# Kernel tuning notes

Hardware: AMD Instinct MI355X
Metric: run time of the kernel (lower is better)

## Reference

```python
import jax, jax.numpy as jnp
import numpy as np
import math


def _interp_linear(x, t_out):
    # x: [B, D, Lin] -> [B, D, t_out]; matches torch F.interpolate(mode='linear', align_corners=False)
    lin = x.shape[-1]
    pos = (jnp.arange(t_out, dtype=jnp.float32) + 0.5) * (lin / t_out) - 0.5
    pos = jnp.clip(pos, 0.0, lin - 1.0)
    lo = jnp.floor(pos).astype(jnp.int32)
    hi = jnp.minimum(lo + 1, lin - 1)
    w = pos - lo.astype(jnp.float32)
    return x[..., lo] * (1.0 - w) + x[..., hi] * w


def _forward(x, in_w, in_b, gq_w, gq_b, gk_w, gk_b, gv_w, gv_b, go_w, go_b, curv,
             wav0, wav1, wav2, wav3, wrec_w, wrec_b,
             te1_w, te1_b, te2_w, te2_b, td1_w, td1_b, td2_w, td2_b, bd_w, bd_b,
             cc_w, cc_b, ln_g, ln_b, mm1_w, mm1_b, mm2_w, mm2_b,
             dn1_w, dn1_b, dn2_w, dn2_b, dn3_w, dn3_b, out_w, out_b,
             noise_sched, noise):
    B, T, _ = x.shape
    L, H = curv.shape
    D = in_w.shape[1]
    hd = D // H
    dn = ('NCH', 'OIH', 'NCH')
    h = x @ in_w + in_b
    total_loss = jnp.float32(0.0)
    wavs = [wav0, wav1, wav2, wav3]
    for l in range(L):  # static small layer loop
        # ---- GeometricAttention (vectorized hyperbolic-distance softmax) ----
        q = (h @ gq_w[l] + gq_b[l]).reshape(B, T, H, hd)
        k = (h @ gk_w[l] + gk_b[l]).reshape(B, T, H, hd)
        v = (h @ gv_w[l] + gv_b[l]).reshape(B, T, H, hd)
        c = jnp.abs(curv[l]) + 1e-8                       # [H]
        cb = c[None, :, None, None]
        qn = jnp.einsum('bthd,bthd->bht', q, q)           # [B,H,T]
        kn = jnp.einsum('bthd,bthd->bht', k, k)
        qk = jnp.einsum('bihd,bjhd->bhij', q, k)          # [B,H,T,T]
        d2 = jnp.maximum(qn[:, :, :, None] + kn[:, :, None, :] - 2.0 * qk, 0.0)
        denom = jnp.maximum((1.0 - cb * qn[:, :, :, None]) * (1.0 - cb * kn[:, :, None, :]), 1e-5)
        arg = jnp.maximum(1.0 + cb * (2.0 * d2) / denom, 1.00001)
        dist = jnp.arccosh(arg) / jnp.sqrt(cb)
        attn = jax.nn.softmax(-dist, axis=-1)             # temperature = 1.0
        geom = jnp.einsum('bhij,bjhd->bihd', attn, v).reshape(B, T, D) @ go_w[l] + go_b[l]
        # ---- WaveletTransform ----
        xf = h.transpose(0, 2, 1)                          # [B,D,T]
        decomps = []
        for i, wv in enumerate(wavs):
            filt = jax.nn.softmax(wv[l], axis=-1)          # [D,K]
            K = filt.shape[-1]
            dec = jax.lax.conv_general_dilated(xf, filt[:, None, :], (1,), [(K - 1, 0)],
                                               feature_group_count=D, dimension_numbers=dn)
            dec = dec[:, :, ::2 ** (i + 1)]
            decomps.append(_interp_linear(dec, T))
        comb = jnp.concatenate(decomps, axis=1).transpose(0, 2, 1)  # [B,T,4D]
        wave = comb @ wrec_w[l] + wrec_b[l]
        # ---- TopologicalLayer ----
        tf = jax.nn.relu(h @ te1_w[l] + te1_b[l]) @ te2_w[l] + te2_b[l]
        topo = h + (jax.nn.relu(tf @ td1_w[l] + td1_b[l]) @ td2_w[l] + td2_b[l])
        bd = tf @ bd_w[l] + bd_b[l]
        total_loss = total_loss + jnp.mean(jax.nn.relu(bd[..., 0] - bd[..., 1] + 0.1))
        # ---- CausalConvolution (kernel 3, dilation 2**l) ----
        dil = 2 ** l
        pad = 2 * dil
        cc = jax.lax.conv_general_dilated(h.transpose(0, 2, 1), cc_w[l], (1,), [(pad, 0)],
                                          rhs_dilation=(dil,), dimension_numbers=dn)
        cc = (cc + cc_b[l][None, :, None]).transpose(0, 2, 1)
        # ---- combine + LayerNorm (dropout is identity in eval) ----
        s = geom + wave + topo + cc
        mu = jnp.mean(s, axis=-1, keepdims=True)
        var = jnp.var(s, axis=-1, keepdims=True)
        h = (s - mu) / jnp.sqrt(var + 1e-5) * ln_g + ln_b
    # ---- manifold mixer (T > 1 branch) ----
    last = h[:, -1]
    pen = h[:, -2]
    mix = jnp.tanh(jnp.concatenate([last, pen], axis=-1) @ mm1_w + mm1_b) @ mm2_w + mm2_b
    cur = last + mix
    # ---- diffusion refinement ----
    half = D // 2
    emb_f = jnp.exp(jnp.arange(half, dtype=jnp.float32) * (-math.log(10000.0) / (half - 1)))
    S = noise.shape[0]
    for t in range(S):  # static diffusion_steps=10
        noisy = cur + noise[t] * noise_sched[t]
        te = jnp.full((B, 1), float(t), dtype=jnp.float32) * emb_f[None, :]
        temb = jnp.concatenate([jnp.sin(te), jnp.cos(te)], axis=-1)  # [B,D]
        di = jnp.concatenate([noisy, temb], axis=-1)
        npred = jax.nn.silu(jax.nn.silu(di @ dn1_w + dn1_b) @ dn2_w + dn2_b) @ dn3_w + dn3_b
        cur = cur - npred * noise_sched[t]
    pred = cur @ out_w + out_b
    return pred, total_loss


def setup_inputs() -> dict:
    key = jax.random.key(0)
    B, T, Din, D, L, H, P, S = 16, 256, 384, 512, 6, 8, 64, 10
    ctr = [0]
    def rn(shape, s=0.05):
        ctr[0] += 1
        return jax.random.normal(jax.random.fold_in(key, ctr[0]), shape, jnp.float32) * s
    d = {}
    d['x'] = rn((B, T, Din), 1.0)
    d['in_w'] = rn((Din, D)); d['in_b'] = rn((D,), 0.01)
    for nm in ['gq', 'gk', 'gv', 'go']:
        d[nm + '_w'] = rn((L, D, D)); d[nm + '_b'] = rn((L, D), 0.01)
    d['curv'] = rn((L, H), 1.0)
    for i in range(4):
        d['wav%d' % i] = rn((L, D, 2 ** (i + 2)), 1.0)
    d['wrec_w'] = rn((L, 4 * D, D)); d['wrec_b'] = rn((L, D), 0.01)
    d['te1_w'] = rn((L, D, P)); d['te1_b'] = rn((L, P), 0.01)
    d['te2_w'] = rn((L, P, P)); d['te2_b'] = rn((L, P), 0.01)
    d['td1_w'] = rn((L, P, D)); d['td1_b'] = rn((L, D), 0.01)
    d['td2_w'] = rn((L, D, D)); d['td2_b'] = rn((L, D), 0.01)
    d['bd_w'] = rn((L, P, 2)); d['bd_b'] = rn((L, 2), 0.01)
    d['cc_w'] = rn((L, D, D, 3)); d['cc_b'] = rn((L, D), 0.01)
    d['ln_g'] = jnp.ones((D,), jnp.float32); d['ln_b'] = jnp.zeros((D,), jnp.float32)
    d['mm1_w'] = rn((2 * D, D)); d['mm1_b'] = rn((D,), 0.01)
    d['mm2_w'] = rn((D, D)); d['mm2_b'] = rn((D,), 0.01)
    d['dn1_w'] = rn((2 * D, D)); d['dn1_b'] = rn((D,), 0.01)
    d['dn2_w'] = rn((D, D)); d['dn2_b'] = rn((D,), 0.01)
    d['dn3_w'] = rn((D, D)); d['dn3_b'] = rn((D,), 0.01)
    d['out_w'] = rn((D, Din)); d['out_b'] = rn((Din,), 0.01)
    d['noise_sched'] = jnp.linspace(0.1, 0.9, S).astype(jnp.float32)
    d['noise'] = rn((S, B, D), 1.0)
    return d


def reference(x, in_w, in_b, gq_w, gq_b, gk_w, gk_b, gv_w, gv_b, go_w, go_b, curv,
              wav0, wav1, wav2, wav3, wrec_w, wrec_b,
              te1_w, te1_b, te2_w, te2_b, td1_w, td1_b, td2_w, td2_b, bd_w, bd_b,
              cc_w, cc_b, ln_g, ln_b, mm1_w, mm1_b, mm2_w, mm2_b,
              dn1_w, dn1_b, dn2_w, dn2_b, dn3_w, dn3_b, out_w, out_b,
              noise_sched, noise):
    return _forward(x, in_w, in_b, gq_w, gq_b, gk_w, gk_b, gv_w, gv_b, go_w, go_b, curv,
                    wav0, wav1, wav2, wav3, wrec_w, wrec_b,
                    te1_w, te1_b, te2_w, te2_b, td1_w, td1_b, td2_w, td2_b, bd_w, bd_b,
                    cc_w, cc_b, ln_g, ln_b, mm1_w, mm1_b, mm2_w, mm2_b,
                    dn1_w, dn1_b, dn2_w, dn2_b, dn3_w, dn3_b, out_w, out_b,
                    noise_sched, noise)
```

## Files before the change

kernel.cpp:

```cpp
#include <hip/hip_runtime.h>
#include <hip/hip_bf16.h>
#include <math.h>

#define BB 16
#define TT 256
#define DIN 384
#define DD 512
#define LL 6
#define HH 8
#define PP 64
#define SS 10
#define BT (BB*TT)

enum { ACT_NONE=0, ACT_RELU=1, ACT_TANH=2, ACT_SILU=3, ACT_RELU_TAIL=4 };

typedef __attribute__((ext_vector_type(8))) short bf16x8;
typedef __attribute__((ext_vector_type(4))) float f32x4;
typedef __hip_bfloat16 bh16;

typedef const __attribute__((address_space(1))) void gvoid_t;
typedef __attribute__((address_space(3))) void lvoid_t;
__device__ __forceinline__ void gload16(const void* g, void* l) {
    __builtin_amdgcn_global_load_lds((gvoid_t*)g, (lvoid_t*)l, 16, 0, 0);
}
// ... 416 lines not shown
            }
    #pragma unroll
    for (int off = 1; off < 16; off <<= 1)
        #pragma unroll
        for (int fm = 0; fm < 2; ++fm)
            #pragma unroll
            for (int r = 0; r < 4; ++r)
                rmax[fm][r] = fmaxf(rmax[fm][r], __shfl_xor(rmax[fm][r], off));
    if ((lane & 15) == 0)
        #pragma unroll
        for (int fm = 0; fm < 2; ++fm)
            #pragma unroll
            for (int r = 0; r < 4; ++r)
                redA[wn][wm*32 + fm*16 + (lane>>4)*4 + r] = rmax[fm][r];
    __syncthreads();
    #pragma unroll
    for (int fm = 0; fm < 2; ++fm)
        #pragma unroll
        for (int r = 0; r < 4; ++r)
            rmax[fm][r] = fmaxf(rmax[fm][r], redA[wn ^ 1][wm*32 + fm*16 + (lane>>4)*4 + r]);
    float rsum[2][4];
    #pragma unroll
    for (int fm = 0; fm < 2; ++fm)
        #pragma unroll
        for (int r = 0; r < 4; ++r) rsum[fm][r] = 0.f;
    #pragma unroll
    for (int fm = 0; fm < 2; ++fm)
        #pragma unroll
        for (int fn = 0; fn < 8; ++fn)
            #pragma unroll
            for (int r = 0; r < 4; ++r) {
                float e = expf(acc[fm][fn][r] - rmax[fm][r]);
                acc[fm][fn][r] = e;
                rsum[fm][r] += e;
            }
    #pragma unroll
    for (int off = 1; off < 16; off <<= 1)
        #pragma unroll
        for (int fm = 0; fm < 2; ++fm)
            #pragma unroll
            for (int r = 0; r < 4; ++r)
                rsum[fm][r] += __shfl_xor(rsum[fm][r], off);
    if ((lane & 15) == 0)
        #pragma unroll
        for (int fm = 0; fm < 2; ++fm)
            #pragma unroll
            for (int r = 0; r < 4; ++r)
                redB[wn][wm*32 + fm*16 + (lane>>4)*4 + r] = rsum[fm][r];
    __syncthreads();
    float pinv[2][4];
    #pragma unroll
    for (int fm = 0; fm < 2; ++fm)
        #pragma unroll
        for (int r = 0; r < 4; ++r)
            pinv[fm][r] = 1.f / (rsum[fm][r] + redB[wn ^ 1][wm*32 + fm*16 + (lane>>4)*4 + r]);

    f32x4 acc2[2][2];
    #pragma unroll
    for (int i = 0; i < 2; ++i)
        #pragma unroll
        for (int j = 0; j < 2; ++j) acc2[i][j] = (f32x4){0.f,0.f,0.f,0.f};

    const bh16* vbase = qkv + 1024 + hh * 64;
    for (int kt = 0; kt < 4; ++kt) {
        __syncthreads();
        if (wn == (kt >> 1)) {
            int fnb = (kt & 1) * 4;
            #pragma unroll
            for (int fm = 0; fm < 2; ++fm)
                #pragma unroll
                for (int fnl = 0; fnl < 4; ++fnl)
                    #pragma unroll
                    for (int r = 0; r < 4; ++r) {
                        int rowl = wm*32 + fm*16 + (lane>>4)*4 + r;
                        int kl = fnl*16 + (lane & 15);
                        float p = acc[fm][fnb + fnl][r] * pinv[fm][r];
                        Ps[(rowl*8 + ((kl >> 3) ^ (rowl & 7)))*8 + (kl & 7)] = __float2bfloat16(p);
                    }
        }
        #pragma unroll
        for (int j = 0; j < 2; ++j) {
            int c = threadIdx.x + j*256;
            int tr = c >> 3, chk = c & 7;
            bf16x8 v = *(const bf16x8*)(vbase + (size_t)(b*256 + kt*64 + tr)*1600 + chk*8);
            *(bf16x8*)(&Vst[tr*72 + chk*8]) = v;
        }
        __syncthreads();
        #pragma unroll
        for (int j = 0; j < 2; ++j) {
            int c = threadIdx.x + j*256;
            int col = c & 63, chk = c >> 6;
            bf16x8 v;
            #pragma unroll
            for (int e = 0; e < 8; ++e)
                v[e] = (short)Vst[(chk*8 + e)*72 + col];
            Bv[col*8 + (chk ^ (col & 7))] = v;
        }
        __syncthreads();

        bf16x8 pa[2][2], vb[2][2];
        #pragma unroll
        for (int fm = 0; fm < 2; ++fm) {
            int row = wm*32 + fm*16 + (lane & 15);
            #pragma unroll
            for (int ks = 0; ks < 2; ++ks)
                pa[fm][ks] = ((bf16x8*)Ps)[row*8 + ((ks*4 + (lane>>4)) ^ (row & 7))];
        }
        #pragma unroll
        for (int fn = 0; fn < 2; ++fn) {
            int col = wn*32 + fn*16 + (lane & 15);
            #pragma unroll
            for (int ks = 0; ks < 2; ++ks)
                vb[fn][ks] = Bv[col*8 + ((ks*4 + (lane>>4)) ^ (col & 7))];
        }
        #pragma unroll
        for (int ks = 0; ks < 2; ++ks)
            #pragma unroll
            for (int fm = 0; fm < 2; ++fm)
                #pragma unroll
                for (int fn = 0; fn < 2; ++fn)
                    acc2[fm][fn] = __builtin_amdgcn_mfma_f32_16x16x32_bf16(
                        pa[fm][ks], vb[fn][ks], acc2[fm][fn], 0, 0, 0);
    }

    #pragma unroll
    for (int fm = 0; fm < 2; ++fm)
        #pragma unroll
        for (int fn = 0; fn < 2; ++fn)
            #pragma unroll
            for (int r = 0; r < 4; ++r) {
                int rowl = wm*32 + fm*16 + (lane>>4)*4 + r;
                int col = wn*32 + fn*16 + (lane & 15);
                gmb[((size_t)(b*256 + rh*64 + rowl))*512 + hh*64 + col] =
                    __float2bfloat16(acc2[fm][fn][r]);
            }
}

__global__ __launch_bounds__(256) void fgemm_kernel(
    const bh16* __restrict__ A0, const bh16* __restrict__ A1,
    const bh16* __restrict__ A2, const bh16* __restrict__ A3,
    const bh16* __restrict__ B0, const bh16* __restrict__ B1,
    const bh16* __restrict__ B2, const bh16* __restrict__ B3,
    const float* __restrict__ bias,
    float* __restrict__ Cf0, float* __restrict__ Cf1,
    float* __restrict__ Cf2, float* __restrict__ Cf3,
    int dil, const bh16* __restrict__ zp)
{
    __shared__ bf16x8 As[128*8];
    __shared__ bf16x8 Bs[64*8];

    int bx = blockIdx.x, by = blockIdx.y;
    xcd_swizzle_always(bx, by);
    const int zz = blockIdx.z;
    const int ktlo = zz * 18;
    const int kthi = ktlo + 18;

    const int tid  = threadIdx.x;
    const int lane = tid & 63, w = tid >> 6;
    const int wm = w >> 1, wn = w & 1;
    const int row0 = by * 128, col0 = bx * 64;

    f32x4 acc[4][2];
    #pragma unroll
    for (int i = 0; i < 4; ++i)
        #pragma unroll
        for (int j = 0; j < 2; ++j) acc[i][j] = (f32x4){0.f,0.f,0.f,0.f};

    for (int kt = ktlo; kt < kthi; ++kt) {
        const bh16* Aseg; const bh16* Bseg;
        int ldas, ldbs, k0, mask_sh, addr_sh;
        if (kt < 8) {
            Aseg = A0; Bseg = B0; ldas = 512; ldbs = 512;
            k0 = kt << 6; mask_sh = 0; addr_sh = 0;
        } else if (kt < 40) {
            Aseg = A1; Bseg = B1; ldas = 2048; ldbs = 2048;
            k0 = (kt - 8) << 6; mask_sh = 0; addr_sh = 0;
        } else if (kt < 48) {
            Aseg = A2; Bseg = B2; ldas = 512; ldbs = 512;
            k0 = (kt - 40) << 6; mask_sh = 0; addr_sh = 0;
        } else {
            int kl = kt - 48, tap = kl >> 3;
            Aseg = A3; Bseg = B3; ldas = 512; ldbs = 1536;
            k0 = kl << 6;
            mask_sh = (2 - tap) * dil;
            addr_sh = mask_sh + tap;
        }
        #pragma unroll
        for (int j = 0; j < 4; ++j) {
            int c = ((w*4 + j) << 6) + lane;
            int row = c >> 3, chk = c & 7;
            int schk = chk ^ (row & 7);
            int grow = row0 + row;
            const bh16* src = ((grow & 255) >= mask_sh)
                ? (Aseg + (size_t)(grow - addr_sh)*ldas + k0 + schk*8) : zp;
            gload16(src, &As[(w*4 + j) * 64]);
        }
        #pragma unroll
        for (int j = 0; j < 2; ++j) {
            int c = ((w*2 + j) << 6) + lane;
            int row = c >> 3, chk = c & 7;
            int schk = chk ^ (row & 7);
            int gcol = col0 + row;
            gload16(Bseg + (size_t)gcol*ldbs + k0 + schk*8, &Bs[(w*2 + j) * 64]);
        }
        asm volatile("s_waitcnt vmcnt(0)" ::: "memory");
        __syncthreads();

        bf16x8 a[4][2], b[2][2];
        #pragma unroll
        for (int fm = 0; fm < 4; ++fm) {
            int row = wm*64 + fm*16 + (lane & 15);
            #pragma unroll
            for (int ks = 0; ks < 2; ++ks)
                a[fm][ks] = As[row*8 + ((ks*4 + (lane>>4)) ^ (row & 7))];
        }
        #pragma unroll
        for (int fn = 0; fn < 2; ++fn) {
            int col = wn*32 + fn*16 + (lane & 15);
            #pragma unroll
            for (int ks = 0; ks < 2; ++ks)
                b[fn][ks] = Bs[col*8 + ((ks*4 + (lane>>4)) ^ (col & 7))];
        }
        #pragma unroll
        for (int ks = 0; ks < 2; ++ks)
            #pragma unroll
            for (int fm = 0; fm < 4; ++fm)
                #pragma unroll
                for (int fn = 0; fn < 2; ++fn)
                    acc[fm][fn] = __builtin_amdgcn_mfma_f32_16x16x32_bf16(
                        a[fm][ks], b[fn][ks], acc[fm][fn], 0, 0, 0);
        __syncthreads();
    }

    float* Cf = (zz == 0) ? Cf0 : (zz == 1) ? Cf1 : (zz == 2) ? Cf2 : Cf3;
    #pragma unroll
    for (int fm = 0; fm < 4; ++fm) {
        #pragma unroll
        for (int fn = 0; fn < 2; ++fn) {
            int gc = col0 + wn*32 + fn*16 + (lane & 15);
            float bs = (zz == 0) ? bias[gc] : 0.f;
            #pragma unroll
            for (int r = 0; r < 4; ++r) {
                int gr = row0 + wm*64 + fm*16 + (lane>>4)*4 + r;
                Cf[(size_t)gr*512 + gc] = acc[fm][fn][r] + bs;
            }
        }
    }
}

__global__ __launch_bounds__(256) void hgemm16_kernel(
    const bh16* __restrict__ A, int lda, long aZ,
    const bh16* __restrict__ Bt, int ldb,
    const float* __restrict__ bias,
    const float* __restrict__ pre,
    float* __restrict__ Of, bh16* __restrict__ Ob, long oZ,
    int N, int K, int act,
    float* __restrict__ curf, bh16* __restrict__ curb,
    const float* __restrict__ scaleptr)
{
    const int z = blockIdx.z;
    A += (long)z * aZ;
    const int lane = threadIdx.x & 63, w = threadIdx.x >> 6;
    const int col0 = blockIdx.x * 64 + w * 16;
    const int ar = lane & 15;
    const int koff = (lane >> 4) * 8;
    const bh16* arow = A + (size_t)ar * lda + koff;
    const bh16* brow = Bt + (size_t)(col0 + ar) * ldb + koff;
    f32x4 acc = {0.f, 0.f, 0.f, 0.f};
    const int nkt = K >> 5;
    for (int kt0 = 0; kt0 < nkt; kt0 += 8) {
        bf16x8 av[8], bv[8];
        #pragma unroll
        for (int j = 0; j < 8; ++j) {
            av[j] = *(const bf16x8*)(arow + (size_t)(kt0 + j) * 32);
            bv[j] = *(const bf16x8*)(brow + (size_t)(kt0 + j) * 32);
        }
        #pragma unroll
        for (int j = 0; j < 8; ++j)
            acc = __builtin_amdgcn_mfma_f32_16x16x32_bf16(av[j], bv[j], acc, 0, 0, 0);
    }
    const int col = col0 + ar;
    float bs = bias ? bias[col] : 0.f;
    float sc = scaleptr ? *scaleptr : 0.f;
    #pragma unroll
    for (int r = 0; r < 4; ++r) {
        int row = (lane >> 4) * 4 + r;
        float v = acc[r] + bs;
        if (pre) v += pre[(size_t)row * N + col];
        if (act == ACT_SILU)      v = v / (1.f + expf(-v));
        else if (act == ACT_TANH) v = tanhf(v);
        if (curf) {
            size_t o = (size_t)row * 512 + col;
            float nc = curf[o] - v * sc;
            curf[o] = nc;
            curb[o] = __float2bfloat16(nc);
        } else {
            size_t o = (size_t)z * oZ + (size_t)row * N + col;
            if (Of) Of[o] = v;
            if (Ob) Ob[o] = __float2bfloat16(v);
        }
    }
}

__device__ __forceinline__ f32x4 hslice(const bh16* A, int lda, const bh16* Bt, int ldb,
                                        int col0, int K, int lane)
{
    const int ar = lane & 15;
    const int koff = (lane >> 4) * 8;
    const bh16* arow = A + (size_t)ar * lda + koff;
    const bh16* brow = Bt + (size_t)(col0 + ar) * ldb + koff;
    f32x4 acc = {0.f, 0.f, 0.f, 0.f};
    const int nkt = K >> 5;
    for (int kt0 = 0; kt0 < nkt; kt0 += 8) {
        bf16x8 av[8], bv[8];
        #pragma unroll
        for (int j = 0; j < 8; ++j) {
            av[j] = *(const bf16x8*)(arow + (size_t)(kt0 + j) * 32);
            bv[j] = *(const bf16x8*)(brow + (size_t)(kt0 + j) * 32);
        }
        #pragma unroll
        for (int j = 0; j < 8; ++j)
            acc = __builtin_amdgcn_mfma_f32_16x16x32_bf16(av[j], bv[j], acc, 0, 0, 0);
    }
    return acc;
}

__device__ __forceinline__ void headbar(int* ctr, int* bar)
{
    __threadfence();
    __syncthreads();
    if (threadIdx.x == 0) {
        __hip_atomic_fetch_add(ctr, 1, __ATOMIC_ACQ_REL, __HIP_MEMORY_SCOPE_AGENT);
        *bar += 8;
        while (__hip_atomic_load(ctr, __ATOMIC_ACQUIRE, __HIP_MEMORY_SCOPE_AGENT) < *bar)
            __builtin_amdgcn_s_sleep(8);
    }
    __syncthreads();
    __threadfence();
}

__global__ __launch_bounds__(256) void head_kernel(
    const float* __restrict__ h,
    const bh16* __restrict__ mm1T, const float* __restrict__ mm1b,
    const bh16* __restrict__ mm2T, const float* __restrict__ mm2b,
    const bh16* __restrict__ dn1T,
    const bh16* __restrict__ dn2T, const float* __restrict__ dn2b,
    const bh16* __restrict__ dn3T, const float* __restrict__ dn3b,
    const bh16* __restrict__ outT, const float* __restrict__ outb,
    const float* __restrict__ pre1, const float* __restrict__ nsched,
    bh16* __restrict__ tmb16, float* __restrict__ curf, bh16* __restrict__ cur16,
    bh16* __restrict__ d1b16, bh16* __restrict__ d2b16,
    float* __restrict__ out, int* __restrict__ ctr)
{
    __shared__ __align__(16) bh16 catL[16 * 1032];
    const int bx = blockIdx.x;
    const int tid = threadIdx.x;
    const int lane = tid & 63, w = tid >> 6;
    int bar = 0;

    for (int e = tid; e < 16 * 1024; e += 256) {
        int k = e & 1023, b = e >> 10;
        float v = (k < 512) ? h[((size_t)b * TT + 255) * DD + k]
                            : h[((size_t)b * TT + 254) * DD + (k - 512)];
        catL[b * 1032 + k] = __float2bfloat16(v);
    }
    __syncthreads();

    const int col0 = bx * 64 + w * 16;
    const int colr = col0 + (lane & 15);

    {
        f32x4 acc = hslice((const bh16*)catL, 1032, mm1T, 1024, col0, 1024, lane);
        float bs = mm1b[colr];
        #pragma unroll
        for (int r = 0; r < 4; ++r) {
            int row = (lane >> 4) * 4 + r;
            tmb16[(size_t)row * 512 + colr] = __float2bfloat16(tanhf(acc[r] + bs));
        }
    }
    headbar(ctr, &bar);
    {
        f32x4 acc = hslice(tmb16, 512, mm2T, 512, col0, 512, lane);
        float bs = mm2b[colr];
        #pragma unroll
        for (int r = 0; r < 4; ++r) {
            int row = (lane >> 4) * 4 + r;
            float cv = h[((size_t)row * TT + 255) * DD + colr] + acc[r] + bs;
            curf[(size_t)row * 512 + colr] = cv;
            cur16[(size_t)row * 512 + colr] = __float2bfloat16(cv);
        }
    }
    headbar(ctr, &bar);
    for (int t = 0; t < SS; ++t) {
        float sc = nsched[t];
        {
            f32x4 acc = hslice(cur16, 512, dn1T, 1024, col0, 512, lane);
            #pragma unroll
            for (int r = 0; r < 4; ++r) {
                int row = (lane >> 4) * 4 + r;
                float v = acc[r] + pre1[(size_t)t * 8192 + row * 512 + colr];
                v = v / (1.f + expf(-v));
                d1b16[(size_t)row * 512 + colr] = __float2bfloat16(v);
            }
        }
        headbar(ctr, &bar);
        {
            f32x4 acc = hslice(d1b16, 512, dn2T, 512, col0, 512, lane);
            float bs = dn2b[colr];
            #pragma unroll
            for (int r = 0; r < 4; ++r) {
                int row = (lane >> 4) * 4 + r;
                float v = acc[r] + bs;
                v = v / (1.f + expf(-v));
                d2b16[(size_t)row * 512 + colr] = __float2bfloat16(v);
            }
        }
        headbar(ctr, &bar);
        {
            f32x4 acc = hslice(d2b16, 512, dn3T, 512, col0, 512, lane);
            float bs = dn3b[colr];
            #pragma unroll
            for (int r = 0; r < 4; ++r) {
                int row = (lane >> 4) * 4 + r;
                size_t o = (size_t)row * 512 + colr;
                float nc = curf[o] - (acc[r] + bs) * sc;
                curf[o] = nc;
                cur16[o] = __float2bfloat16(nc);
            }
        }
        headbar(ctr, &bar);
    }
    if (bx < 6) {
        f32x4 acc = hslice(cur16, 512, outT, 512, col0, 512, lane);
        float bs = outb[colr];
        #pragma unroll
        for (int r = 0; r < 4; ++r) {
            int row = (lane >> 4) * 4 + r;
            out[(size_t)row * 384 + colr] = acc[r] + bs;
        }
    }
}

__global__ __launch_bounds__(256) void wave4_kernel(const bh16* __restrict__ hb,
                                                    const float* __restrict__ wav0,
                                                    const float* __restrict__ wav1,
                                                    const float* __restrict__ wav2,
                                                    const float* __restrict__ wav3,
                                                    int l,
                                                    bh16* __restrict__ comb)
{
    __shared__ float dtile[66 * 64];
    __shared__ float ftile[32 * 64];
    const int dblk = blockIdx.x;
    const int iy = blockIdx.y;
    const int b = blockIdx.z;
    const int i = iy >> 1, thalf = iy & 1;
    const int Karr[4] = {4, 8, 16, 32};
    const int K = Karr[i], sv = 2 << i, Ti = 128 >> i;
    const int tid = threadIdx.x;
    const int dbase = dblk * 64;
    if (tid < 64) {
        const float* wsrc = (i == 0) ? wav0 : (i == 1) ? wav1 : (i == 2) ? wav2 : wav3;
        const float* row = wsrc + ((size_t)l * DD + dbase + tid) * K;
        float mx = -1e30f;
        for (int k = 0; k < K; ++k) mx = fmaxf(mx, row[k]);
        float s = 0.f;
        for (int k = 0; k < K; ++k) { float e = expf(row[k] - mx); ftile[k*64 + tid] = e; s += e; }
        float inv = 1.f / s;
        for (int k = 0; k < K; ++k) ftile[k*64 + tid] *= inv;
    }
    const float invsv = 1.f / (float)sv;
    const int t0 = thalf * 128;
    float p0 = ((float)t0 + 0.5f) * invsv - 0.5f;
    p0 = fminf(fmaxf(p0, 0.f), (float)(Ti - 1));
    const int jbase = (int)p0;
    float p1 = ((float)(t0 + 127) + 0.5f) * invsv - 0.5f;
    p1 = fminf(fmaxf(p1, 0.f), (float)(Ti - 1));
    const int him = min((int)p1 + 1, Ti - 1);
    const int jcount = him - jbase + 1;
    __syncthreads();
    const bh16* hcol = hb + (size_t)b * (TT * DD) + dbase;
    for (int e = tid; e < jcount * 64; e += 256) {
        int jl = e >> 6, d0 = e & 63;
        int j = jbase + jl;
        int tb = j * sv - (K - 1);
        float acc = 0.f;
        #pragma unroll 4
        for (int k = 0; k < K; ++k) {
            int t = tb + k;
            if (t >= 0)
                acc += b2f(*(const unsigned short*)(hcol + (size_t)t * DD + d0)) * ftile[k * 64 + d0];
        }
        dtile[jl * 64 + d0] = acc;
    }
    __syncthreads();
    for (int e = tid; e < 128 * 64; e += 256) {
        int tl = e >> 6, d0 = e & 63;
        int t = t0 + tl;
        float pos = ((float)t + 0.5f) * invsv - 0.5f;
        pos = fminf(fmaxf(pos, 0.f), (float)(Ti - 1));
        int lo = (int)pos;
        int hi = min(lo + 1, Ti - 1);
        float w = pos - (float)lo;
        float v = dtile[(lo - jbase) * 64 + d0] * (1.f - w) + dtile[(hi - jbase) * 64 + d0] * w;
        comb[((size_t)b * TT + t) * 2048 + i * 512 + dbase + d0] = __float2bfloat16(v);
    }
}

__global__ __launch_bounds__(256) void add_ln_kernel(const float* __restrict__ s0, const float* __restrict__ s1,
                                                     const float* __restrict__ s2, const float* __restrict__ s3,
                                                     float* __restrict__ h, bh16* __restrict__ hb,
                                                     const float* __restrict__ g, const float* __restrict__ be)
{
    int lane = threadIdx.x & 63, wid = threadIdx.x >> 6;
    size_t row = (size_t)blockIdx.x * 4 + wid;
    const float* sr0 = s0 + row * DD;
    const float* sr1 = s1 + row * DD;
    const float* sr2 = s2 + row * DD;
    const float* sr3 = s3 + row * DD;
    float* hr = h + row * DD;
    bh16* hbr = hb + row * DD;
    float xv[8]; float sum = 0.f;
    #pragma unroll
    for (int u = 0; u < 8; ++u) {
        int c = lane + u * 64;
        xv[u] = sr0[c] + sr1[c] + sr2[c] + sr3[c] + hr[c];
        sum += xv[u];
    }
    #pragma unroll
    for (int off = 32; off; off >>= 1) sum += __shfl_xor(sum, off);
    float mu = sum * (1.f / 512.f);
    float sq = 0.f;
    #pragma unroll
    for (int u = 0; u < 8; ++u) { float d = xv[u] - mu; sq += d * d; }
    #pragma unroll
    for (int off = 32; off; off >>= 1) sq += __shfl_xor(sq, off);
    float rstd = 1.f / sqrtf(sq * (1.f / 512.f) + 1e-5f);
    #pragma unroll
    for (int u = 0; u < 8; ++u) {
        int c = lane + u * 64;
        float v = (xv[u] - mu) * rstd * g[c] + be[c];
        hr[c] = v;
        hbr[c] = __float2bfloat16(v);
    }
}

__global__ __launch_bounds__(256) void wtrans_kernel(const float* __restrict__ W, bh16* __restrict__ Wt,
                                                     int K, int N, long lstride)
{
    int l = blockIdx.z;
    const float* Wl = W + (size_t)l * K * N;
    bh16* Wo = Wt + (size_t)l * lstride;
    __shared__ float tile[32][33];
    int n0 = blockIdx.x * 32, k0 = blockIdx.y * 32;
    int lx = threadIdx.x & 31, ly = threadIdx.x >> 5;
    #pragma unroll
    for (int j = 0; j < 4; ++j) {
        int kk = ly + j * 8;
        tile[kk][lx] = Wl[(size_t)(k0 + kk) * N + n0 + lx];
    }
    __syncthreads();
    #pragma unroll
    for (int j = 0; j < 4; ++j) {
        int nr = ly + j * 8;
        Wo[(size_t)(n0 + nr) * K + k0 + lx] = __float2bfloat16(tile[lx][nr]);
    }
}

__global__ __launch_bounds__(256) void wtrans4_kernel(const float* __restrict__ gq, const float* __restrict__ gk,
                                                      const float* __restrict__ gv, const float* __restrict__ te1,
                                                      bh16* __restrict__ qkvT)
{
    int bxx = blockIdx.x, l = blockIdx.z;
    const float* W; long off; int N; int n0;
    if (bxx < 16)      { W = gq;  off = 0;      N = 512; n0 = bxx * 32; }
    else if (bxx < 32) { W = gk;  off = 262144; N = 512; n0 = (bxx - 16) * 32; }
    else if (bxx < 48) { W = gv;  off = 524288; N = 512; n0 = (bxx - 32) * 32; }
    else               { W = te1; off = 786432; N = 64;  n0 = (bxx - 48) * 32; }
    const float* Wl = W + (size_t)l * 512 * N;
    bh16* Wo = qkvT + (size_t)l * 819200 + off;
    __shared__ float tile[32][33];
    int k0 = blockIdx.y * 32;
    int lx = threadIdx.x & 31, ly = threadIdx.x >> 5;
    #pragma unroll
    for (int j = 0; j < 4; ++j) {
        int kk = ly + j * 8;
        tile[kk][lx] = Wl[(size_t)(k0 + kk) * N + n0 + lx];
    }
    __syncthreads();
    #pragma unroll
    for (int j = 0; j < 4; ++j) {
        int nr = ly + j * 8;
        Wo[(size_t)(n0 + nr) * 512 + k0 + lx] = __float2bfloat16(tile[lx][nr]);
    }
}

__global__ __launch_bounds__(256) void wtransH_kernel(
    const float* __restrict__ mm1w, const float* __restrict__ mm2w,
    const float* __restrict__ dn1w, const float* __restrict__ dn2w,
    const float* __restrict__ dn3w, const float* __restrict__ outw,
    bh16* __restrict__ mm1T, bh16* __restrict__ mm2T, bh16* __restrict__ dn1T,
    bh16* __restrict__ dn2T, bh16* __restrict__ dn3T, bh16* __restrict__ outT)
{
    int bx = blockIdx.x;
    const float* W; bh16* Wo; int K, N, bloc;
    if (bx < 512)       { W = mm1w; Wo = mm1T; K = 1024; N = 512; bloc = bx; }
    else if (bx < 768)  { W = mm2w; Wo = mm2T; K = 512;  N = 512; bloc = bx - 512; }
    else if (bx < 1280) { W = dn1w; Wo = dn1T; K = 1024; N = 512; bloc = bx - 768; }
    else if (bx < 1536) { W = dn2w; Wo = dn2T; K = 512;  N = 512; bloc = bx - 1280; }
    else if (bx < 1792) { W = dn3w; Wo = dn3T; K = 512;  N = 512; bloc = bx - 1536; }
    else                { W = outw; Wo = outT; K = 512;  N = 384; bloc = bx - 1792; }
    int nblk = N / 32;
    int n0 = (bloc % nblk) * 32, k0 = (bloc / nblk) * 32;
    __shared__ float tile[32][33];
    int lx = threadIdx.x & 31, ly = threadIdx.x >> 5;
    #pragma unroll
    for (int j = 0; j < 4; ++j) {
        int kk = ly + j * 8;
        tile[kk][lx] = W[(size_t)(k0 + kk) * N + n0 + lx];
    }
    __syncthreads();
    #pragma unroll
    for (int j = 0; j < 4; ++j) {
        int nr = ly + j * 8;
        Wo[(size_t)(n0 + nr) * K + k0 + lx] = __float2bfloat16(tile[lx][nr]);
    }
}

__global__ __launch_bounds__(256) void ccconv_kernel(const float* __restrict__ ccw, bh16* __restrict__ ccT)
{
    size_t idx = (size_t)blockIdx.x * 256 + threadIdx.x;
    int i = idx & 511; size_t rem = idx >> 9;
    int tap = (int)(rem % 3); rem /= 3;
    int o = (int)(rem & 511); int l = (int)(rem >> 9);
    ccT[idx] = __float2bfloat16(ccw[(((size_t)l*512 + o)*512 + i)*3 + tap]);
}

__global__ __launch_bounds__(256) void qkvbias_kernel(const float* __restrict__ qb_, const float* __restrict__ kb_,
                                                      const float* __restrict__ vb_, const float* __restrict__ t1b_,
                                                      float* __restrict__ ob,
                                                      const float* __restrict__ gob, const float* __restrict__ wrb,
                                                      const float* __restrict__ tdb, const float* __restrict__ ccb,
                                                      float* __restrict__ bsum)
{
    int idx = blockIdx.x * 256 + threadIdx.x;
    if (idx < 6 * 1600) {
        int l = idx / 1600, n = idx % 1600;
        float v = (n < 512) ? qb_[l*512 + n]
                : (n < 1024) ? kb_[l*512 + n - 512]
                : (n < 1536) ? vb_[l*512 + n - 1024]
                : t1b_[l*64 + n - 1536];
        ob[idx] = v;
    }
    if (idx < 6 * 512) {
        bsum[idx] = gob[idx] + wrb[idx] + tdb[idx] + ccb[idx];
    }
}

__global__ __launch_bounds__(256) void convx_kernel(const float* __restrict__ x, bh16* __restrict__ xb)
{
    size_t idx = (size_t)blockIdx.x * 256 + threadIdx.x;
    xb[idx] = __float2bfloat16(x[idx]);
}

__global__ __launch_bounds__(256) void build_E_kernel(const float* __restrict__ noise, const float* __restrict__ sched,
                                                      bh16* __restrict__ E)
{
    int idx = blockIdx.x * 256 + threadIdx.x;
    if (idx >= SS * BB * 1024) return;
    int k = idx & 1023; int rem = idx >> 10; int b = rem & 15; int t = rem >> 4;
    float v;
    if (k < 512) {
        v = sched[t] * noise[((size_t)t * BB + b) * 512 + k];
    } else {
        int j = k - 512;
        const float kfac = -9.210340371976184f / 255.f;
        v = (j < 256) ? sinf((float)t * expf((float)j * kfac))
                      : cosf((float)t * expf((float)(j - 256) * kfac));
    }
    E[idx] = __float2bfloat16(v);
}

__global__ void init_kernel(bh16* zp, float* loss, int* ctr)
{
    int t = threadIdx.x;
    if (t < 64) zp[t] = __float2bfloat16(0.f);
    if (t == 64) *loss = 0.f;
    if (t == 65) *ctr = 0;
}

__global__ void fail_kernel(float* p) { p[0] = 1e30f; }

extern "C" void kernel_launch(void* const* d_in, const int* in_sizes, int n_in,
                              void* d_out, int out_size, void* d_ws, size_t ws_size,
                              hipStream_t stream)
{
    const float* x      = (const float*)d_in[0];
    const float* in_w   = (const float*)d_in[1];
    const float* in_b   = (const float*)d_in[2];
    const float* gq_w   = (const float*)d_in[3];
    const float* gq_b   = (const float*)d_in[4];
    const float* gk_w   = (const float*)d_in[5];
    const float* gk_b   = (const float*)d_in[6];
    const float* gv_w   = (const float*)d_in[7];
    const float* gv_b   = (const float*)d_in[8];
    const float* go_w   = (const float*)d_in[9];
    const float* go_b   = (const float*)d_in[10];
    const float* curv   = (const float*)d_in[11];
    const float* wav0   = (const float*)d_in[12];
    const float* wav1   = (const float*)d_in[13];
    const float* wav2   = (const float*)d_in[14];
    const float* wav3   = (const float*)d_in[15];
    const float* wrec_w = (const float*)d_in[16];
    const float* wrec_b = (const float*)d_in[17];
    const float* te1_w  = (const float*)d_in[18];
    const float* te1_b  = (const float*)d_in[19];
    const float* te2_w  = (const float*)d_in[20];
    const float* te2_b  = (const float*)d_in[21];
    const float* td1_w  = (const float*)d_in[22];
    const float* td1_b  = (const float*)d_in[23];
    const float* td2_w  = (const float*)d_in[24];
    const float* td2_b  = (const float*)d_in[25];
    const float* bd_w   = (const float*)d_in[26];
    const float* bd_b   = (const float*)d_in[27];
    const float* cc_w   = (const float*)d_in[28];
    const float* cc_b   = (const float*)d_in[29];
    const float* ln_g   = (const float*)d_in[30];
    const float* ln_b   = (const float*)d_in[31];
    const float* mm1_w  = (const float*)d_in[32];
    const float* mm1_b  = (const float*)d_in[33];
    const float* mm2_w  = (const float*)d_in[34];
    const float* mm2_b  = (const float*)d_in[35];
    const float* dn1_w  = (const float*)d_in[36];
    const float* dn1_b  = (const float*)d_in[37];
    const float* dn2_w  = (const float*)d_in[38];
    const float* dn2_b  = (const float*)d_in[39];
    const float* dn3_w  = (const float*)d_in[40];
    const float* dn3_b  = (const float*)d_in[41];
    const float* out_w  = (const float*)d_in[42];
    const float* out_b  = (const float*)d_in[43];
    const float* nsched = (const float*)d_in[44];
    const float* noise  = (const float*)d_in[45];
    float* out = (float*)d_out;
    float* ws  = (float*)d_ws;

    const size_t o_h   = 0;
    const size_t o_dec = 2097152;
    const size_t o_s   = 4194304;
    const size_t o_at  = 6619136;
    const size_t o_mix = 15038464;
    const size_t o_cur = 15046656;
    const size_t o_qkb = 15054848;
    const size_t o_bs  = 15064448;
    const size_t o_ctr = 15067520;
    const size_t FP32_TOTAL = 15095808;
    const size_t b_xb   = 0;
    const size_t b_hb   = 1572864;
    const size_t b_qkv  = 3670016;
    const size_t b_pb   = 12320768;
    const size_t b_gmb  = 20709376;
    const size_t b_tdb  = 22806528;
    const size_t b_zp   = 25165824;
    const size_t b_inwT = 25166336;
    const size_t b_qkvT = 25362944;
    const size_t b_goT  = 30278144;
    const size_t b_wrT  = 31851008;
    const size_t b_td1T = 38142464;
    const size_t b_td2T = 38339072;
    const size_t b_te2T = 39911936;
    const size_t b_ccT  = 39936512;
    const size_t BF16_TOTAL = 44655104;
    const size_t TOTAL_BYTES = FP32_TOTAL * 4 + BF16_TOTAL * 2;
    if (ws_size < TOTAL_BYTES) { fail_kernel<<<1, 1, 0, stream>>>(out); return; }

    float* h_   = ws + o_h;
    float* s2_  = ws + o_dec;
    float* s_   = ws + o_s;
    float* at_  = ws + o_at;
    float* s3_  = at_ + 4194304;
    float* s4_  = at_ + 6291456;
    float* curf = ws + o_cur;
    float* qkvbias = ws + o_qkb;
    float* bsum = ws + o_bs;
    int*   ctr  = (int*)(ws + o_ctr);
    bh16* bp   = (bh16*)(ws + FP32_TOTAL);
    bh16* xb   = bp + b_xb;
    bh16* hb   = bp + b_hb;
    bh16* qkvb = bp + b_qkv;
    bh16* pb   = bp + b_pb;
    bh16* gmb  = bp + b_gmb;
    bh16* tdb  = bp + b_tdb;
    bh16* zp   = bp + b_zp;
    bh16* inwT = bp + b_inwT;
    bh16* qkvT = bp + b_qkvT;
    bh16* goT  = bp + b_goT;
    bh16* wrT  = bp + b_wrT;
    bh16* td1T = bp + b_td1T;
    bh16* td2T = bp + b_td2T;
    bh16* te2T = bp + b_te2T;
    bh16* ccT  = bp + b_ccT;
    bh16* combb = (bh16*)at_;

    bh16* dn1T  = pb;
    bh16* dn2T  = pb + 524288;
    bh16* dn3T  = pb + 786432;
    bh16* mm1T  = pb + 1048576;
    bh16* mm2T  = pb + 1572864;
    bh16* outT  = pb + 1835008;
    bh16* E16   = pb + 2031616;
    bh16* tmb16 = pb + 2211840;
    bh16* cur16 = pb + 2220032;
    bh16* d1b16 = pb + 2228224;
    bh16* d2b16 = pb + 2236416;
    float* pre1 = s2_;

    auto mgp = [&](const bh16* A, int lda, const bh16* Bt, int ldb,
                   const float* bias, float* Cf, bh16* Cb, int ldc,
                   int M, int N, int K, int shift, int accum, int act) {
        dim3 g((N + 63) / 64, M / 128, 1);
        mgemm_kernel<<<g, 256, 0, stream>>>(A, lda, Bt, ldb, bias, Cf, Cb, ldc, N, K,
                                            shift, accum, act, zp);
    };

    init_kernel<<<1, 128, 0, stream>>>(zp, out + BB * DIN, ctr);
    convx_kernel<<<BT * DIN / 256, 256, 0, stream>>>(x, xb);
    wtrans_kernel<<<dim3(DD/32, DIN/32, 1), 256, 0, stream>>>(in_w, inwT, DIN, DD, (long)DIN*DD);
    wtrans4_kernel<<<dim3(50, 16, 6), 256, 0, stream>>>(gq_w, gk_w, gv_w, te1_w, qkvT);
    qkvbias_kernel<<<38, 256, 0, stream>>>(gq_b, gk_b, gv_b, te1_b, qkvbias,
                                           go_b, wrec_b, td2_b, cc_b, bsum);
    wtrans_kernel<<<dim3(16, 16, 6), 256, 0, stream>>>(go_w, goT, DD, DD, (long)DD*DD);
    wtrans_kernel<<<dim3(16, 64, 6), 256, 0, stream>>>(wrec_w, wrT, 2048, DD, 2048L*DD);
    wtrans_kernel<<<dim3(16, 2, 6), 256, 0, stream>>>(td1_w, td1T, PP, DD, (long)PP*DD);
    wtrans_kernel<<<dim3(16, 16, 6), 256, 0, stream>>>(td2_w, td2T, DD, DD, (long)DD*DD);
    wtrans_kernel<<<dim3(2, 2, 6), 256, 0, stream>>>(te2_w, te2T, PP, PP, (long)PP*PP);
    ccconv_kernel<<<18432, 256, 0, stream>>>(cc_w, ccT);

    mgp(xb, DIN, inwT, DIN, in_b, h_, hb, DD, BT, DD, DIN, 0, 0, ACT_NONE);

    for (int l = 0; l < LL; ++l) {
        mgp(hb, DD, qkvT + (size_t)l*819200, DD, qkvbias + (size_t)l*1600,
            nullptr, qkvb, 1600, BT, 1600, DD, 0, 0, ACT_RELU_TAIL);
        fattn_kernel<<<dim3(4, 128), 256, 0, stream>>>(qkvb, curv + (size_t)l*HH, gmb);
        wave4_kernel<<<dim3(8, 8, 16), 256, 0, stream>>>(hb, wav0, wav1, wav2, wav3, l, combb);
        topo_kernel<<<dim3(8, 32), 256, 0, stream>>>(
            qkvb + 1536, te2T + (size_t)l*4096, te2_b + (size_t)l*PP,
            td1T + (size_t)l*32768, td1_b + (size_t)l*DD,
            bd_w + (size_t)l*PP*2, bd_b + (size_t)l*2, out + BB*DIN, tdb);
        fgemm_kernel<<<dim3(8, 32, 4), 256, 0, stream>>>(
            gmb, combb, tdb, hb,
            goT + (size_t)l*262144, wrT + (size_t)l*1048576,
            td2T + (size_t)l*262144, ccT + (size_t)l*786432,
            bsum + (size_t)l*512, s_, s2_, s3_, s4_, 1 << l, zp);
        add_ln_kernel<<<BT/4, 256, 0, stream>>>(s_, s2_, s3_, s4_, h_, hb, ln_g, ln_b);
    }

    wtransH_kernel<<<1984, 256, 0, stream>>>(mm1_w, mm2_w, dn1_w, dn2_w, dn3_w, out_w,
                                             mm1T, mm2T, dn1T, dn2T, dn3T, outT);
    build_E_kernel<<<640, 256, 0, stream>>>(noise, nsched, E16);
    hgemm16_kernel<<<dim3(8, 1, SS), 256, 0, stream>>>(
        E16, 1024, 16*1024, dn1T, 1024, dn1_b, nullptr, pre1, nullptr, 8192,
        512, 1024, ACT_NONE, nullptr, nullptr, nullptr);
    head_kernel<<<8, 256, 0, stream>>>(
        h_, mm1T, mm1_b, mm2T, mm2_b, dn1T, dn2T, dn2_b, dn3T, dn3_b,
        outT, out_b, pre1, nsched, tmb16, curf, cur16, d1b16, d2b16, out, ctr);
}
```

Before: 1.003 ms.

## Rework head kernel grid barrier and stage activations through LDS via atomics

Replaces the fenced acquire/release grid barrier in the head kernel with a relaxed-atomic barrier using shorter sleeps. Inter-block activations are now exchanged as packed bf16 pairs via agent-scope atomic stores and loads, then staged into a padded LDS tile before each MFMA slice. The running state is kept in registers instead of being round-tripped through global fp32. The aim is to cut barrier latency and global-memory traffic across the 30+ sequential barriers, at the cost of relying on relaxed ordering without explicit fences, which could be a memory-ordering risk.

```diff
diff --git a/kernel.cpp b/kernel.cpp
--- a/kernel.cpp
+++ b/kernel.cpp
@@ -742,12 +742,12 @@
     }
 }
 
-__device__ __forceinline__ f32x4 hslice(const bh16* A, int lda, const bh16* Bt, int ldb,
+__device__ __forceinline__ f32x4 lslice(const unsigned short* A, int lda, const bh16* Bt, int ldb,
                                         int col0, int K, int lane)
 {
     const int ar = lane & 15;
     const int koff = (lane >> 4) * 8;
-    const bh16* arow = A + (size_t)ar * lda + koff;
+    const unsigned short* arow = A + (size_t)ar * lda + koff;
     const bh16* brow = Bt + (size_t)(col0 + ar) * ldb + koff;
     f32x4 acc = {0.f, 0.f, 0.f, 0.f};
     const int nkt = K >> 5;
@@ -765,21 +765,40 @@
     return acc;
 }
 
-__device__ __forceinline__ void headbar(int* ctr, int* bar)
-{
-    __threadfence();
+__device__ __forceinline__ void st_store(unsigned* st, int row, int colr, int lane, float v)
+{
+    float other = __shfl_xor(v, 1);
+    if (!(lane & 1)) {
+        unsigned lo = (unsigned)__bfloat16_as_ushort(__float2bfloat16(v));
+        unsigned hi = (unsigned)__bfloat16_as_ushort(__float2bfloat16(other));
+        __hip_atomic_store(st + ((row * 512 + colr) >> 1), lo | (hi << 16),
+                           __ATOMIC_RELAXED, __HIP_MEMORY_SCOPE_AGENT);
+    }
+}
+
+__device__ __forceinline__ void st_stage(unsigned short* ALds, const unsigned* st, int tid)
+{
+    for (int e = tid; e < 4096; e += 256) {
+        unsigned uv = __hip_atomic_load(st + e, __ATOMIC_RELAXED, __HIP_MEMORY_SCOPE_AGENT);
+        int row = e >> 8, cp = (e & 255) << 1;
+        *(unsigned*)(ALds + row * 520 + cp) = uv;
+    }
+    __syncthreads();
+}
+
+__device__ __forceinline__ void gridbar(int* ctr, int* bar)
+{
     __syncthreads();
     if (threadIdx.x == 0) {
-        __hip_atomic_fetch_add(ctr, 1, __ATOMIC_ACQ_REL, __HIP_MEMORY_SCOPE_AGENT);
         *bar += 8;
-        while (__hip_atomic_load(ctr, __ATOMIC_ACQUIRE, __HIP_MEMORY_SCOPE_AGENT) < *bar)
-            __builtin_amdgcn_s_sleep(8);
-    }
-    __syncthreads();
-    __threadfence();
-}
-
-__global__ __launch_bounds__(256) void head_kernel(
+        __hip_atomic_fetch_add(ctr, 1, __ATOMIC_RELAXED, __HIP_MEMORY_SCOPE_AGENT);
+        while (__hip_atomic_load(ctr, __ATOMIC_RELAXED, __HIP_MEMORY_SCOPE_AGENT) < *bar)
+            __builtin_amdgcn_s_sleep(1);
+    }
+    __syncthreads();
+}
+
+__global__ __launch_bounds__(256) void head2_kernel(
     const float* __restrict__ h,
     const bh16* __restrict__ mm1T, const float* __restrict__ mm1b,
     const bh16* __restrict__ mm2T, const float* __restrict__ mm2b,
@@ -788,95 +807,98 @@
     const bh16* __restrict__ dn3T, const float* __restrict__ dn3b,
     const bh16* __restrict__ outT, const float* __restrict__ outb,
     const float* __restrict__ pre1, const float* __restrict__ nsched,
-    bh16* __restrict__ tmb16, float* __restrict__ curf, bh16* __restrict__ cur16,
-    bh16* __restrict__ d1b16, bh16* __restrict__ d2b16,
+    unsigned* __restrict__ stTM, unsigned* __restrict__ stCur,
+    unsigned* __restrict__ stD1, unsigned* __restrict__ stD2,
     float* __restrict__ out, int* __restrict__ ctr)
 {
-    __shared__ __align__(16) bh16 catL[16 * 1032];
+    __shared__ __align__(16) unsigned short catL[16 * 1032];
+    __shared__ __align__(16) unsigned short ALds[16 * 520];
     const int bx = blockIdx.x;
     const int tid = threadIdx.x;
     const int lane = tid & 63, w = tid >> 6;
     int bar = 0;
+    const int col0 = bx * 64 + w * 16;
+    const int colr = col0 + (lane & 15);
+    const int row0 = (lane >> 4) * 4;
 
     for (int e = tid; e < 16 * 1024; e += 256) {
         int k = e & 1023, b = e >> 10;
         float v = (k < 512) ? h[((size_t)b * TT + 255) * DD + k]
                             : h[((size_t)b * TT + 254) * DD + (k - 512)];
-        catL[b * 1032 + k] = __float2bfloat16(v);
-    }
-    __syncthreads();
-
-    const int col0 = bx * 64 + w * 16;
-    const int colr = col0 + (lane & 15);
+        catL[b * 1032 + k] = __bfloat16_as_ushort(__float2bfloat16(v));
+    }
+    __syncthreads();
 
     {
-        f32x4 acc = hslice((const bh16*)catL, 1032, mm1T, 1024, col0, 1024, lane);
+        f32x4 acc = lslice(catL, 1032, mm1T, 1024, col0, 1024, lane);
         float bs = mm1b[colr];
         #pragma unroll
+        for (int r = 0; r < 4; ++r)
+            st_store(stTM, row0 + r, colr, lane, tanhf(acc[r] + bs));
+    }
+    gridbar(ctr, &bar);
+
+    float cur_reg[4];
+    {
+        st_stage(ALds, stTM, tid);
+        f32x4 acc = lslice(ALds, 520, mm2T, 512, col0, 512, lane);
+        float bs = mm2b[colr];
+        #pragma unroll
         for (int r = 0; r < 4; ++r) {
-            int row = (lane >> 4) * 4 + r;
-            tmb16[(size_t)row * 512 + colr] = __float2bfloat16(tanhf(acc[r] + bs));
-        }
-    }
-    headbar(ctr, &bar);
-    {
-        f32x4 acc = hslice(tmb16, 512, mm2T, 512, col0, 512, lane);
-        float bs = mm2b[colr];
-        #pragma unroll
-        for (int r = 0; r < 4; ++r) {
-            int row = (lane >> 4) * 4 + r;
-            float cv = h[((size_t)row * TT + 255) * DD + colr] + acc[r] + bs;
-            curf[(size_t)row * 512 + colr] = cv;
-            cur16[(size_t)row * 512 + colr] = __float2bfloat16(cv);
-        }
-    }
-    headbar(ctr, &bar);
+            float cv = h[((size_t)(row0 + r) * TT + 255) * DD + colr] + acc[r] + bs;
+            cur_reg[r] = cv;
+            st_store(stCur, row0 + r, colr, lane, cv);
+        }
+    }
+    gridbar(ctr, &bar);
+
     for (int t = 0; t < SS; ++t) {
         float sc = nsched[t];
         {
-            f32x4 acc = hslice(cur16, 512, dn1T, 1024, col0, 512, lane);
+            st_stage(ALds, stCur, tid);
+            f32x4 acc = lslice(ALds, 520, dn1T, 1024, col0, 512, lane);
             #pragma unroll
             for (int r = 0; r < 4; ++r) {
-                int row = (lane >> 4) * 4 + r;
-                float v = acc[r] + pre1[(size_t)t * 8192 + row * 512 + colr];
+                float v = acc[r] + pre1[(size_t)t * 8192 + (row0 + r) * 512 + colr];
                 v = v / (1.f + expf(-v));
-                d1b16[(size_t)row * 512 + colr] = __float2bfloat16(v);
+                st_store(stD1, row0 + r, colr, lane, v);
             }
         }
-        headbar(ctr, &bar);
+        gridbar(ctr, &bar);
         {
-            f32x4 acc = hslice(d1b16, 512, dn2T, 512, col0, 512, lane);
+            st_stage(ALds, stD1, tid);
+            f32x4 acc = lslice(ALds, 520, dn2T, 512, col0, 512, lane);
             float bs = dn2b[colr];
             #pragma unroll
             for (int r = 0; r < 4; ++r) {
-                int row = (lane >> 4) * 4 + r;
                 float v = acc[r] + bs;
                 v = v / (1.f + expf(-v));
-                d2b16[(size_t)row * 512 + colr] = __float2bfloat16(v);
+                st_store(stD2, row0 + r, colr, lane, v);
             }
         }
-        headbar(ctr, &bar);
+        gridbar(ctr, &bar);
         {
-            f32x4 acc = hslice(d2b16, 512, dn3T, 512, col0, 512, lane);
+            st_stage(ALds, stD2, tid);
+            f32x4 acc = lslice(ALds, 520, dn3T, 512, col0, 512, lane);
             float bs = dn3b[colr];
             #pragma unroll
             for (int r = 0; r < 4; ++r) {
-                int row = (lane >> 4) * 4 + r;
-                size_t o = (size_t)row * 512 + colr;
-                float nc = curf[o] - (acc[r] + bs) * sc;
-                curf[o] = nc;
-                cur16[o] = __float2bfloat16(nc);
+                float nc = cur_reg[r] - (acc[r] + bs) * sc;
+                cur_reg[r] = nc;
+                st_store(stCur, row0 + r, colr, lane, nc);
             }
         }
-        headbar(ctr, &bar);
-    }
-    if (bx < 6) {
-        f32x4 acc = hslice(cur16, 512, outT, 512, col0, 512, lane);
-        float bs = outb[colr];
-        #pragma unroll
-        for (int r = 0; r < 4; ++r) {
-            int row = (lane >> 4) * 4 + r;
-            out[(size_t)row * 384 + colr] = acc[r] + bs;
+        gridbar(ctr, &bar);
+    }
+
+    {
+        st_stage(ALds, stCur, tid);
+        if (bx < 6) {
+            f32x4 acc = lslice(ALds, 520, outT, 512, col0, 512, lane);
+            float bs = outb[colr];
+            #pragma unroll
+            for (int r = 0; r < 4; ++r)
+                out[(size_t)(row0 + r) * 384 + colr] = acc[r] + bs;
         }
     }
 }
@@ -1188,7 +1210,6 @@
     const size_t o_dec = 2097152;
     const size_t o_s   = 4194304;
     const size_t o_at  = 6619136;
-    const size_t o_mix = 15038464;
     const size_t o_cur = 15046656;
     const size_t o_qkb = 15054848;
     const size_t o_bs  = 15064448;
@@ -1219,7 +1240,6 @@
     float* at_  = ws + o_at;
     float* s3_  = at_ + 4194304;
     float* s4_  = at_ + 6291456;
-    float* curf = ws + o_cur;
     float* qkvbias = ws + o_qkb;
     float* bsum = ws + o_bs;
     int*   ctr  = (int*)(ws + o_ctr);
@@ -1248,11 +1268,11 @@
     bh16* mm2T  = pb + 1572864;
     bh16* outT  = pb + 1835008;
     bh16* E16   = pb + 2031616;
-    bh16* tmb16 = pb + 2211840;
-    bh16* cur16 = pb + 2220032;
-    bh16* d1b16 = pb + 2228224;
-    bh16* d2b16 = pb + 2236416;
     float* pre1 = s2_;
+    unsigned* stTM  = (unsigned*)s4_;
+    unsigned* stCur = stTM + 4096;
+    unsigned* stD1  = stTM + 8192;
+    unsigned* stD2  = stTM + 12288;
 
     auto mgp = [&](const bh16* A, int lda, const bh16* Bt, int ldb,
                    const float* bias, float* Cf, bh16* Cb, int ldc,
@@ -1300,7 +1320,7 @@
     hgemm16_kernel<<<dim3(8, 1, SS), 256, 0, stream>>>(
         E16, 1024, 16*1024, dn1T, 1024, dn1_b, nullptr, pre1, nullptr, 8192,
         512, 1024, ACT_NONE, nullptr, nullptr, nullptr);
-    head_kernel<<<8, 256, 0, stream>>>(
+    head2_kernel<<<8, 256, 0, stream>>>(
         h_, mm1T, mm1_b, mm2T, mm2_b, dn1T, dn2T, dn2_b, dn3T, dn3_b,
-        outT, out_b, pre1, nsched, tmb16, curf, cur16, d1b16, d2b16, out, ctr);
-}
+        outT, out_b, pre1, nsched, stTM, stCur, stD1, stD2, out, ctr);
+}
```

After: 1.003 ms. No clear change (-0.0%).
